# Optimization experiments

Measured on AMD Instinct MI355X. Metric: run time of the kernel, lower is better.

Reference implementation:

```python
import jax, jax.numpy as jnp
import numpy as np

N = 100000   # nodes
E = 1600000  # edges
H = 128      # hidden_dim
B = 4096     # number of root pairs
HOPS = 3


def setup_inputs() -> dict:
    key = jax.random.key(0)
    ks = jax.random.split(key, 12)
    s = 0.05
    return {
        "node_feat": jax.random.normal(ks[0], (N, H), jnp.float32),
        "send_embd": jax.random.normal(ks[1], (N, H), jnp.float32),
        "edge_index": jax.random.randint(ks[2], (2, E), 0, N, dtype=jnp.int32),
        "root_index": jax.random.randint(ks[3], (2 * B,), 0, N, dtype=jnp.int32),
        "agg_by_source": 1,
        "lin1_W": jax.random.normal(ks[4], (2 * H, H), jnp.float32) * s,
        "lin1_b": jnp.zeros((H,), jnp.float32),
        "gat_W": jax.random.normal(ks[5], (HOPS, H, H), jnp.float32) * s,
        "gat_asrc": jax.random.normal(ks[6], (HOPS, H), jnp.float32) * s,
        "gat_adst": jax.random.normal(ks[7], (HOPS, H), jnp.float32) * s,
        "gat_b": jnp.zeros((HOPS, H), jnp.float32),
        "lstm_Wih": jax.random.normal(ks[8], (HOPS, 2 * H, 4 * H), jnp.float32) * s,
        "lstm_Whh": jax.random.normal(ks[9], (HOPS, H, 4 * H), jnp.float32) * s,
        "lstm_b": jnp.zeros((HOPS, 4 * H), jnp.float32),
        "lin2_W": jax.random.normal(ks[10], (H, H), jnp.float32) * s,
        "lin2_b": jnp.zeros((H,), jnp.float32),
    }


def _gat_breadth(x, src, dst, W, a_src, a_dst, b):
    # GATConv(heads=1) followed by tanh (GeniePath Breadth layer)
    xw = x @ W                                  # [N, H]
    e_score = jax.nn.leaky_relu((xw @ a_src)[src] + (xw @ a_dst)[dst], 0.2)  # [E]
    # softmax over incoming edges of each destination node
    m = jax.ops.segment_max(e_score, dst, num_segments=N)
    ex = jnp.exp(e_score - m[dst])
    z = jax.ops.segment_sum(ex, dst, num_segments=N)
    alpha = ex / z[dst]                          # [E]
    agg = jax.ops.segment_sum(alpha[:, None] * xw[src], dst, num_segments=N)
    return jnp.tanh(agg + b)


def _lstm_step(inp, h, c, Wih, Whh, b):
    gates = inp @ Wih + h @ Whh + b              # [N, 4H]
    i, f, g, o = jnp.split(gates, 4, axis=-1)
    c = jax.nn.sigmoid(f) * c + jax.nn.sigmoid(i) * jnp.tanh(g)
    h = jax.nn.sigmoid(o) * jnp.tanh(c)
    return h, c


def reference(node_feat, send_embd, edge_index, root_index, agg_by_source,
              lin1_W, lin1_b, gat_W, gat_asrc, gat_adst, gat_b,
              lstm_Wih, lstm_Whh, lstm_b, lin2_W, lin2_b):
    src, dst = edge_index[0], edge_index[1]
    # Aggregation stage input: concat node embedding with broadcast embedding
    x = jnp.concatenate([node_feat, send_embd], axis=1) @ lin1_W + lin1_b  # [N, H]
    # GeniePathLazy: all breadth (GAT) layers run on the projected input x
    h_tmps = [
        _gat_breadth(x, src, dst, gat_W[i], gat_asrc[i], gat_adst[i], gat_b[i])
        for i in range(HOPS)
    ]
    # Depth: per-node LSTM over the hop axis, input = cat(h_tmp, x_prev)
    h = jnp.zeros_like(x)
    c = jnp.zeros_like(x)
    xs = x
    for i in range(HOPS):
        inp = jnp.concatenate([h_tmps[i], xs], axis=1)   # [N, 2H]
        h, c = _lstm_step(inp, h, c, lstm_Wih[i], lstm_Whh[i], lstm_b[i])
        xs = h
    out = xs @ lin2_W + lin2_b                            # [N, H]
    roots = root_index.reshape(-1, 2)
    src_nodes = roots[:, 0] if agg_by_source else roots[:, 1]
    return out[src_nodes]                                 # [B, H]
```

## Files before the change

### kernel.cpp

```cpp
#include <hip/hip_runtime.h>

constexpr int N  = 100000;
constexpr int E  = 1600000;
constexpr int H  = 128;
constexpr int NB = 4096;
constexpr int HOPS = 3;
constexpr int EPT = 8;

constexpr int WOFF_L1  = 0;
constexpr int WOFF_GAT = 32768;
constexpr int WOFF_CAT = 81920;
constexpr int WOFF_L2  = 671744;
constexpr int WTOT     = 688128;

constexpr size_t ALIGN = 256;
constexpr size_t alup(size_t x) { return (x + ALIGN - 1) & ~(ALIGN - 1); }

constexpr size_t OFF_X       = 0;
constexpr size_t OFF_SSRC    = alup(OFF_X + (size_t)N * H * 4);
constexpr size_t OFF_SDST    = alup(OFF_SSRC + (size_t)3 * N * 4);
constexpr size_t OFF_WVEC    = alup(OFF_SDST + (size_t)3 * N * 4);
constexpr size_t OFF_SELMAP  = alup(OFF_WVEC + 6 * H * 4);
constexpr size_t OFF_NODELST = alup(OFF_SELMAP + (size_t)N * 4);
constexpr size_t OFF_CNT     = alup(OFF_NODELST + NB * 4);
constexpr size_t OFF_DEG     = alup(OFF_CNT + 256);
constexpr size_t OFF_OFFS    = alup(OFF_DEG + NB * 4);
constexpr size_t OFF_CURSOR  = alup(OFF_OFFS + (NB + 1) * 4);
constexpr size_t OFF_ESORT   = alup(OFF_CURSOR + NB * 4);
constexpr size_t OFF_AGGXH   = alup(OFF_ESORT + (size_t)E * 4);
constexpr size_t OFF_AGGXL   = alup(OFF_AGGXH + (size_t)3 * NB * H * 2);
constexpr size_t OFF_XSH     = alup(OFF_AGGXL + (size_t)3 * NB * H * 2);
constexpr size_t OFF_XSL     = alup(OFF_XSH + (size_t)NB * H * 2);
constexpr size_t OFF_L2OUT   = alup(OFF_XSL + (size_t)NB * H * 2);
constexpr size_t OFF_WHI     = alup(OFF_L2OUT + (size_t)NB * H * 4);
constexpr size_t OFF_WLO     = alup(OFF_WHI + (size_t)WTOT * 2);

constexpr size_t OFF_AGGRAW  = OFF_X;
constexpr size_t OFF_WV2     = OFF_X + (size_t)16 * 1024 * 1024;
constexpr size_t OFF_C2      = OFF_WV2 + 6 * 256 * 4;

__device__ __forceinline__ float lrelu(float v) { return v > 0.f ? v : 0.2f * v; }
__device__ __forceinline__ float sigmoidf_(float v) { return 1.f / (1.f + __expf(-v)); }

__device__ __forceinline__ unsigned short f2bf(float f) {
  unsigned u = __float_as_uint(f);
  unsigned r = (u + 0x7FFFu + ((u >> 16) & 1u)) >> 16;
  return (unsigned short)r;
}
__device__ __forceinline__ float bf2f(unsigned short h) {
  return __uint_as_float((unsigned)h << 16);
}
__device__ __forceinline__ void split_rne(float f, unsigned short& hi, unsigned short& lo) {
  unsigned short hh = f2bf(f);
  hi = hh;
  lo = f2bf(f - bf2f(hh));
}
__device__ __forceinline__ void split_trunc(float f, short* hi, short* lo) {
  unsigned u = __float_as_uint(f);
  *hi = (short)(u >> 16);
  float r = f - __uint_as_float(u & 0xFFFF0000u);
  *lo = (short)(__float_as_uint(r) >> 16);
}

typedef short bf16x8 __attribute__((ext_vector_type(8)));
typedef float f32x4  __attribute__((ext_vector_type(4)));

#define MFMA3(ACC, AH, AL, BH, BL)                                               \
  ACC = __builtin_amdgcn_mfma_f32_16x16x32_bf16(AH, BH, ACC, 0, 0, 0);           \
  ACC = __builtin_amdgcn_mfma_f32_16x16x32_bf16(AH, BL, ACC, 0, 0, 0);           \
  ACC = __builtin_amdgcn_mfma_f32_16x16x32_bf16(AL, BH, ACC, 0, 0, 0);

__global__ void init_ws(int* __restrict__ sel_map, int* __restrict__ deg,
                        int* __restrict__ cursor, int* __restrict__ cnt,
                        int* __restrict__ need_flag) {
  int i = blockIdx.x * 256 + threadIdx.x;
  int stride = gridDim.x * 256;
  for (int n = i; n < N; n += stride) { sel_map[n] = -1; need_flag[n] = 0; }
  for (int n = i; n < NB; n += stride) { deg[n] = 0; cursor[n] = 0; }
  if (i < 64) cnt[i] = 0;
}

__global__ void prep_kernel(const float* __restrict__ gat_W,
                            const float* __restrict__ a_src,
                            const float* __restrict__ a_dst,
                            float* __restrict__ wvec,
                            const float* __restrict__ lin1_W,
                            const float* __restrict__ Wih,
                            const float* __restrict__ Whh,
                            const float* __restrict__ lin2_W,
                            unsigned short* __restrict__ whi,
                            unsigned short* __restrict__ wlo) {
  if (blockIdx.x < 6) {
    int i = blockIdx.x >> 1, which = blockIdx.x & 1;
    int k = threadIdx.x;
    __shared__ float av[H];
    if (k < H) av[k] = which ? a_dst[i * H + k] : a_src[i * H + k];
    __syncthreads();
    if (k >= H) return;
    const float* Wr = gat_W + (size_t)i * H * H + (size_t)k * H;
    float s = 0.f;
    #pragma unroll 8
    for (int j = 0; j < H; j++) s = fmaf(Wr[j], av[j], s);
    wvec[(i * 2 + which) * H + k] = s;
    return;
  }
  int idx = (blockIdx.x - 6) * 256 + threadIdx.x;
  if (idx >= WTOT) return;
  float v;
  if (idx < WOFF_GAT) {
    int rel = idx;
    int e = rel & 7, lane = (rel >> 3) & 63, tile = rel >> 9;
    int nl = lane & 15, quad = lane >> 4;
    int c = tile & 7, t = tile >> 3;
    int n = c * 16 + nl, k = t * 32 + quad * 8 + e;
    v = lin1_W[k * 128 + n];
  } else if (idx < WOFF_CAT) {
    int rel = idx - WOFF_GAT;
    int hop = rel / 16384; rel %= 16384;
    int e = rel & 7, lane = (rel >> 3) & 63, tile = rel >> 9;
    int nl = lane & 15, quad = lane >> 4;
    int c = tile & 7, t = tile >> 3;
    int n = c * 16 + nl, k = t * 32 + quad * 8 + e;
    v = gat_W[hop * 16384 + k * 128 + n];
  } else if (idx < WOFF_L2) {
    int rel = idx - WOFF_CAT;
    int hop = rel / 196608; rel %= 196608;
    int e = rel & 7, lane = (rel >> 3) & 63, tile = rel >> 9;
    int nl = lane & 15, quad = lane >> 4;
    int c = tile & 31, t = tile >> 5;
    int ftile = c >> 2, g = c & 3;
    int col = g * 128 + ftile * 16 + nl;
    int k = t * 32 + quad * 8 + e;
    v = (k < 256) ? Wih[hop * 131072 + k * 512 + col]
                  : Whh[hop * 65536 + (k - 256) * 512 + col];
  } else {
    int rel = idx - WOFF_L2;
    int e = rel & 7, lane = (rel >> 3) & 63, tile = rel >> 9;
    int nl = lane & 15, quad = lane >> 4;
    int c = tile & 7, t = tile >> 3;
    int n = c * 16 + nl, k = t * 32 + quad * 8 + e;
    v = lin2_W[k * 128 + n];
  }
  unsigned short hh, ll;
  split_rne(v, hh, ll);
  whi[idx] = hh;
  wlo[idx] = ll;
}

__global__ void prep2_kernel(const float* __restrict__ lin1_W,
                             const float* __restrict__ lin1_b,
                             const float* __restrict__ wvec,
                             float* __restrict__ wv2, float* __restrict__ c2) {
  int v = blockIdx.x;
  int j = threadIdx.x;
  __shared__ float wv[H];
  if (j < H) wv[j] = wvec[v * H + j];
  __syncthreads();
  const float* Wr = lin1_W + (size_t)j * H;
  float s = 0.f;
  #pragma unroll 8
  for (int m = 0; m < H; m++) s = fmaf(Wr[m], wv[m], s);
  wv2[v * 256 + j] = s;
  if (j == 0) {
    float cc = 0.f;
    for (int m = 0; m < H; m++) cc = fmaf(lin1_b[m], wv[m], cc);
    c2[v] = cc;
  }
}

__global__ void roots_assign(const int* __restrict__ root, const int* __restrict__ aggp,
                             int* __restrict__ sel_map, int* __restrict__ node_list,
                             int* __restrict__ cnt, int* __restrict__ need_flag) {
  int b = blockIdx.x * 256 + threadIdx.x;
  if (b >= NB) return;
  int node = root[2 * b + (aggp[0] ? 0 : 1)];
  need_flag[node] = 1;
  int old = atomicCAS(&sel_map[node], -1, -2);
  if (old == -1) {
    int c = atomicAdd(cnt, 1);
    sel_map[node] = c;
    node_list[c] = node;
  }
}

__global__ void count_edges(const int* __restrict__ ei, const int* __restrict__ sel_map,
                            int* __restrict__ deg) {
  const int T = gridDim.x * 256;
  const int base = blockIdx.x * 256 + threadIdx.x;
  int dn[EPT];
  #pragma unroll
  for (int k = 0; k < EPT; k++) {
    int e = base + k * T;
    dn[k] = (e < E) ? ei[E + e] : -1;
  }
  #pragma unroll
  for (int k = 0; k < EPT; k++) {
    if (dn[k] >= 0) dn[k] = sel_map[dn[k]];
  }
  #pragma unroll
  for (int k = 0; k < EPT; k++) {
    if (dn[k] >= 0) atomicAdd(&deg[dn[k]], 1);
  }
}

__global__ __launch_bounds__(1024)
void scan_kernel(const int* __restrict__ deg, int* __restrict__ offs) {
  __shared__ int part[1024];
  int t = threadIdx.x;
  int base = t * 4;
  int v0 = deg[base], v1 = deg[base + 1], v2 = deg[base + 2], v3 = deg[base + 3];
  int s = v0 + v1 + v2 + v3;
  part[t] = s;
  __syncthreads();
  for (int off = 1; off < 1024; off <<= 1) {
    int tmp = (t >= off) ? part[t - off] : 0;
    __syncthreads();
    part[t] += tmp;
    __syncthreads();
  }
  int run = part[t] - s;
  offs[base] = run; run += v0;
  offs[base + 1] = run; run += v1;
  offs[base + 2] = run; run += v2;
  offs[base + 3] = run;
  if (t == 1023) offs[NB] = part[1023];
}

__global__ void scatter_edges2(const int* __restrict__ ei, const int* __restrict__ sel_map,
                               const int* __restrict__ offs, int* __restrict__ cursor,
                               int* __restrict__ es_sorted, int* __restrict__ need_flag) {
  const int T = gridDim.x * 256;
  const int base = blockIdx.x * 256 + threadIdx.x;
  int dn[EPT], sn[EPT];
  #pragma unroll
  for (int k = 0; k < EPT; k++) {
    int e = base + k * T;
    dn[k] = (e < E) ? ei[E + e] : -1;
  }
  #pragma unroll
  for (int k = 0; k < EPT; k++) {
    if (dn[k] >= 0) dn[k] = sel_map[dn[k]];
  }
  #pragma unroll
  for (int k = 0; k < EPT; k++) {
    int e = base + k * T;
    if (dn[k] >= 0) sn[k] = ei[e];
  }
  #pragma unroll
  for (int k = 0; k < EPT; k++) {
    if (dn[k] >= 0) {
      int p = atomicAdd(&cursor[dn[k]], 1);
      es_sorted[offs[dn[k]] + p] = sn[k];
      need_flag[sn[k]] = 1;
    }
  }
}

__global__ void compact_need(const int* __restrict__ need_flag,
                             int* __restrict__ need_list, int* __restrict__ need_cnt) {
  int i = blockIdx.x * 256 + threadIdx.x;
  bool f = (i < N) && (need_flag[i] != 0);
  unsigned long long mask = __ballot(f);
  int lane = threadIdx.x & 63;
  int wcnt = __popcll(mask);
  int base = 0;
  if (lane == 0 && wcnt > 0) base = atomicAdd(need_cnt, wcnt);
  base = __shfl(base, 0);
  if (f) {
    int prefix = __popcll(mask & ((1ull << lane) - 1ull));
    need_list[base + prefix] = i;
  }
}

__global__ __launch_bounds__(256)
void score_pass(const float* __restrict__ a0, const float* __restrict__ a1,
                const float* __restrict__ wv2, const float* __restrict__ c2,
                float* __restrict__ s_src, float* __restrict__ s_dst,
                const int* __restrict__ need_list, const int* __restrict__ need_cnt) {
  const int nneed = need_cnt[0];
  if (blockIdx.x * 16 >= nneed) return;
  __shared__ float Ws[6 * 256];
  __shared__ float C2s[6];
  const int t = threadIdx.x, lane = t & 63, wave = t >> 6;
  const int nl = lane & 15;
  #pragma unroll
  for (int v = 0; v < 6; v++) Ws[v * 256 + t] = wv2[v * 256 + t];
  if (t < 6) C2s[t] = c2[t];
  __syncthreads();

  int r = blockIdx.x * 16 + wave * 4 + (lane >> 4);
  int row = (r < nneed) ? need_list[r] : -1;
  int rc = (row < 0) ? 0 : row;
  const float* src = (nl < 8) ? (a0 + (size_t)rc * H + nl * 16)
                              : (a1 + (size_t)rc * H + (nl - 8) * 16);
  float4 va[4];
  #pragma unroll
  for (int q = 0; q < 4; q++) va[q] = ((const float4*)src)[q];

  float p[6] = {0.f, 0.f, 0.f, 0.f, 0.f, 0.f};
  #pragma unroll
  for (int q = 0; q < 4; q++) {
    float4 v4 = va[q];
    #pragma unroll
    for (int v = 0; v < 6; v++) {
      float4 w4 = *(const float4*)&Ws[v * 256 + nl * 16 + q * 4];
      p[v] = fmaf(v4.x, w4.x, p[v]);
      p[v] = fmaf(v4.y, w4.y, p[v]);
      p[v] = fmaf(v4.z, w4.z, p[v]);
      p[v] = fmaf(v4.w, w4.w, p[v]);
    }
  }
  #pragma unroll
  for (int m = 1; m < 16; m <<= 1)
    #pragma unroll
    for (int v = 0; v < 6; v++) p[v] += __shfl_xor(p[v], m);
  if (nl == 0 && row >= 0) {
    #pragma unroll
    for (int h3 = 0; h3 < 3; h3++) {
      s_src[h3 * N + row] = p[2 * h3 + 0] + C2s[2 * h3 + 0];
      s_dst[h3 * N + row] = p[2 * h3 + 1] + C2s[2 * h3 + 1];
    }
  }
}

__global__ __launch_bounds__(256)
void gat_node_kernel(const int* __restrict__ node_list, const int* __restrict__ cntp,
                     const int* __restrict__ offs, const int* __restrict__ es_sorted,
                     const float* __restrict__ a0, const float* __restrict__ a1,
                     const float* __restrict__ s_src, const float* __restrict__ s_dst,
                     float* __restrict__ agg_raw) {
  int c = blockIdx.x;
  if (c >= cntp[0]) return;
  int t = threadIdx.x;
  int n = node_list[c];
  float sd0 = s_dst[0 * N + n], sd1 = s_dst[1 * N + n], sd2 = s_dst[2 * N + n];
  int e0 = offs[c], e1 = offs[c + 1];
  float m0 = -1e30f, m1 = -1e30f, m2 = -1e30f;
  for (int e = e0 + t; e < e1; e += 256) {
    int s = es_sorted[e];
    m0 = fmaxf(m0, lrelu(s_src[0 * N + s] + sd0));
    m1 = fmaxf(m1, lrelu(s_src[1 * N + s] + sd1));
    m2 = fmaxf(m2, lrelu(s_src[2 * N + s] + sd2));
  }
  __shared__ float red[3][256];
  red[0][t] = m0; red[1][t] = m1; red[2][t] = m2;
  __syncthreads();
  for (int s2 = 128; s2 > 0; s2 >>= 1) {
    if (t < s2) {
      red[0][t] = fmaxf(red[0][t], red[0][t + s2]);
      red[1][t] = fmaxf(red[1][t], red[1][t + s2]);
      red[2][t] = fmaxf(red[2][t], red[2][t + s2]);
    }
    __syncthreads();
  }
  m0 = red[0][0]; m1 = red[1][0]; m2 = red[2][0];
  float u0 = 0.f, u1 = 0.f, u2 = 0.f, z0 = 0.f, z1 = 0.f, z2 = 0.f;
  for (int e = e0; e < e1; e++) {
    int s = es_sorted[e];
    float xs = (t < 128) ? a0[(size_t)s * H + t] : a1[(size_t)s * H + (t - 128)];
    float ex0 = __expf(lrelu(s_src[0 * N + s] + sd0) - m0);
    float ex1 = __expf(lrelu(s_src[1 * N + s] + sd1) - m1);
    float ex2 = __expf(lrelu(s_src[2 * N + s] + sd2) - m2);
    z0 += ex0; z1 += ex1; z2 += ex2;
    u0 = fmaf(ex0, xs, u0); u1 = fmaf(ex1, xs, u1); u2 = fmaf(ex2, xs, u2);
  }
  size_t cb = (size_t)c * 256 + t;
  bool any = e1 > e0;
  agg_raw[0 * ((size_t)NB * 256) + cb] = any ? u0 / z0 : 0.f;
  agg_raw[1 * ((size_t)NB * 256) + cb] = any ? u1 / z1 : 0.f;
  agg_raw[2 * ((size_t)NB * 256) + cb] = any ? u2 / z2 : 0.f;
}

__global__ __launch_bounds__(256)
void gemm_unified(const float* __restrict__ agg_raw,
                  const float* __restrict__ a0, const float* __restrict__ a1,
                  const int* __restrict__ node_list, const int* __restrict__ cntp,
                  const int* __restrict__ offs,
                  const unsigned short* __restrict__ Bth,
                  const unsigned short* __restrict__ Btl,
                  const float* __restrict__ bias,
                  unsigned short* __restrict__ aggxh, unsigned short* __restrict__ aggxl,
                  unsigned short* __restrict__ xsh, unsigned short* __restrict__ xsl) {
  const int t = threadIdx.x, lane = t & 63, wave = t >> 6;
  const int nl = lane & 15, quad = lane >> 4;
  const int rt = blockIdx.x * 64 + wave * 16;
  const int cnt = cntp[0];

  int gr = rt + nl;
  const float *pA, *pB;
  if (gr < 12288) {
    pA = agg_raw + (size_t)gr * 256;
    pB = pA + 128;
  } else {
    int cc = gr - 12288;
    int node = (cc < cnt) ? node_list[cc] : 0;
    pA = a0 + (size_t)node * H;
    pB = a1 + (size_t)node * H;
  }

  f32x4 acc[8];
  #pragma unroll
  for (int c = 0; c < 8; c++) acc[c] = (f32x4){0.f, 0.f, 0.f, 0.f};

  #pragma unroll
  for (int kt = 0; kt < 8; kt++) {
    const float* p = ((kt < 4) ? pA : pB) + (kt & 3) * 32 + quad * 8;
    bf16x8 ahi, alo;
    {
      float4 v0 = *(const float4*)p;
      float4 v1 = *(const float4*)(p + 4);
      float af[8] = {v0.x, v0.y, v0.z, v0.w, v1.x, v1.y, v1.z, v1.w};
      #pragma unroll
      for (int j = 0; j < 8; j++) {
        short h_, l_;
        split_trunc(af[j], &h_, &l_);
        ahi[j] = h_;
        alo[j] = l_;
      }
    }
    #pragma unroll
    for (int c = 0; c < 8; c++) {
      size_t boff = ((size_t)(kt * 8 + c) * 64 + lane) * 8;
      bf16x8 bh = *(const bf16x8*)(Bth + boff);
      bf16x8 bl = *(const bf16x8*)(Btl + boff);
      MFMA3(acc[c], ahi, alo, bh, bl);
    }
  }

  float bv[8];
  #pragma unroll
  for (int c = 0; c < 8; c++) bv[c] = bias[c * 16 + nl];

  #pragma unroll
  for (int r = 0; r < 4; r++) {
    int g2 = rt + quad * 4 + r;
    if (g2 < 12288) {
      int cc = g2 & 4095, h = g2 >> 12;
      bool he = offs[cc + 1] > offs[cc];
      size_t base = (size_t)h * NB * H + (size_t)cc * H;
      #pragma unroll
      for (int c = 0; c < 8; c++) {
        float val = acc[c][r] + (he ? bv[c] : 0.f);
        unsigned short vh, vl;
        split_rne(val, vh, vl);
        aggxh[base + c * 16 + nl] = vh;
        aggxl[base + c * 16 + nl] = vl;
      }
    } else {
      int cc = g2 - 12288;
      size_t base = (size_t)cc * H;
      #pragma unroll
      for (int c = 0; c < 8; c++) {
        float val = acc[c][r] + bv[c];
        unsigned short vh, vl;
        split_rne(val, vh, vl);
        xsh[base + c * 16 + nl] = vh;
        xsl[base + c * 16 + nl] = vl;
      }
    }
  }
}

__global__ __launch_bounds__(512)
void hops3_fused(const unsigned short* __restrict__ aggxh,
                 const unsigned short* __restrict__ aggxl,
                 const unsigned short* __restrict__ xsh,
                 const unsigned short* __restrict__ xsl,
                 const unsigned short* __restrict__ gWh_all,
                 const unsigned short* __restrict__ gWl_all,
                 const float* __restrict__ gbias_all,
                 const unsigned short* __restrict__ CWh_all,
                 const unsigned short* __restrict__ CWl_all,
                 const float* __restrict__ lbias_all,
                 const unsigned short* __restrict__ L2h,
                 const unsigned short* __restrict__ L2l,
                 const float* __restrict__ lin2_b, float* __restrict__ l2out) {
  __shared__ unsigned short Ah[16 * 136], Al[16 * 136];
  __shared__ unsigned short Xh[16 * 136], Xl[16 * 136];
  __shared__ unsigned short Th[16 * 136], Tl[16 * 136];
  __shared__ unsigned short Hh[16 * 136], Hl[16 * 136];
  const int t = threadIdx.x, lane = t & 63, wave = t >> 6;
  const int nl = lane & 15, quad = lane >> 4;
  const int r0 = blockIdx.x * 16;

  for (int i = t; i < 16 * 64; i += 512) {
    int row = i >> 6, c2 = (i & 63) * 2;
    *(ushort2*)&Xh[row * 136 + c2] = *(const ushort2*)&xsh[(size_t)(r0 + row) * H + c2];
    *(ushort2*)&Xl[row * 136 + c2] = *(const ushort2*)&xsl[(size_t)(r0 + row) * H + c2];
  }

  float creg[4] = {0.f, 0.f, 0.f, 0.f};
  const int f = wave * 16 + nl;

  f32x4 acc2[4];
  #pragma unroll
  for (int hop = 0; hop < 3; hop++) {
    const unsigned short* agh = aggxh + (size_t)hop * NB * H;
    const unsigned short* agl = aggxl + (size_t)hop * NB * H;
    __syncthreads();
    for (int i = t; i < 16 * 64; i += 512) {
      int row = i >> 6, c2 = (i & 63) * 2;
      *(ushort2*)&Ah[row * 136 + c2] = *(const ushort2*)&agh[(size_t)(r0 + row) * H + c2];
      *(ushort2*)&Al[row * 136 + c2] = *(const ushort2*)&agl[(size_t)(r0 + row) * H + c2];
    }
    __syncthreads();

    const unsigned short* gWh = gWh_all + hop * 16384;
    const unsigned short* gWl = gWl_all + hop * 16384;
    f32x4 acc1 = (f32x4){0.f, 0.f, 0.f, 0.f};
    #pragma unroll
    for (int kt = 0; kt < 4; kt++) {
      int kk = kt * 32 + quad * 8;
      bf16x8 ah = *(const bf16x8*)&Ah[nl * 136 + kk];
      bf16x8 al = *(const bf16x8*)&Al[nl * 136 + kk];
      size_t boff = ((size_t)(kt * 8 + wave) * 64 + lane) * 8;
      bf16x8 bh = *(const bf16x8*)(gWh + boff);
      bf16x8 bl = *(const bf16x8*)(gWl + boff);
      MFMA3(acc1, ah, al, bh, bl);
    }
    {
      float bv = gbias_all[hop * H + f];
      #pragma unroll
      for (int r = 0; r < 4; r++) {
        int rl = quad * 4 + r;
        float v = tanhf(acc1[r] + bv);
        unsigned short vh, vl2;
        split_rne(v, vh, vl2);
        Th[rl * 136 + f] = vh;
        Tl[rl * 136 + f] = vl2;
      }
    }
    __syncthreads();

    const unsigned short* CWh = CWh_all + hop * 196608;
    const unsigned short* CWl = CWl_all + hop * 196608;
    #pragma unroll
    for (int g = 0; g < 4; g++) acc2[g] = (f32x4){0.f, 0.f, 0.f, 0.f};
    #pragma unroll
    for (int kt = 0; kt < 4; kt++) {
      int kk = kt * 32 + quad * 8;
      bf16x8 ah = *(const bf16x8*)&Th[nl * 136 + kk];
      bf16x8 al = *(const bf16x8*)&Tl[nl * 136 + kk];
      #pragma unroll
      for (int g = 0; g < 4; g++) {
        size_t boff = ((size_t)(kt * 32 + wave * 4 + g) * 64 + lane) * 8;
        bf16x8 bh = *(const bf16x8*)(CWh + boff);
        bf16x8 bl = *(const bf16x8*)(CWl + boff);
        MFMA3(acc2[g], ah, al, bh, bl);
      }
    }
    #pragma unroll
    for (int kt = 0; kt < 4; kt++) {
      int kk = kt * 32 + quad * 8;
      bf16x8 ah, al;
      if (hop == 0) {
        ah = *(const bf16x8*)&Xh[nl * 136 + kk];
        al = *(const bf16x8*)&Xl[nl * 136 + kk];
      } else {
        ah = *(const bf16x8*)&Hh[nl * 136 + kk];
        al = *(const bf16x8*)&Hl[nl * 136 + kk];
      }
      #pragma unroll
      for (int g = 0; g < 4; g++) {
        size_t boff = ((size_t)((kt + 4) * 32 + wave * 4 + g) * 64 + lane) * 8;
        bf16x8 bh = *(const bf16x8*)(CWh + boff);
        bf16x8 bl = *(const bf16x8*)(CWl + boff);
        MFMA3(acc2[g], ah, al, bh, bl);
      }
      if (hop > 0) {
        #pragma unroll
        for (int g = 0; g < 4; g++) {
          size_t boff = ((size_t)((kt + 8) * 32 + wave * 4 + g) * 64 + lane) * 8;
          bf16x8 bh = *(const bf16x8*)(CWh + boff);
          bf16x8 bl = *(const bf16x8*)(CWl + boff);
          MFMA3(acc2[g], ah, al, bh, bl);
        }
      }
    }
    __syncthreads();

    {
      const float* lb = lbias_all + hop * 512;
      float b_i = lb[0 * 128 + f], b_f = lb[1 * 128 + f];
      float b_g = lb[2 * 128 + f], b_o = lb[3 * 128 + f];
      #pragma unroll
      for (int r = 0; r < 4; r++) {
        int rl = quad * 4 + r;
        float gi = acc2[0][r] + b_i;
        float gf = acc2[1][r] + b_f;
        float gg = acc2[2][r] + b_g;
        float go = acc2[3][r] + b_o;
        float cn = sigmoidf_(gf) * creg[r] + sigmoidf_(gi) * tanhf(gg);
        float hn = sigmoidf_(go) * tanhf(cn);
        creg[r] = cn;
        unsigned short vh, vl2;
        split_rne(hn, vh, vl2);
        Hh[rl * 136 + f] = vh;
        Hl[rl * 136 + f] = vl2;
      }
    }
  }
  __syncthreads();

  f32x4 acc3 = (f32x4){0.f, 0.f, 0.f, 0.f};
  #pragma unroll
  for (int kt = 0; kt < 4; kt++) {
    int kk = kt * 32 + quad * 8;
    bf16x8 ah = *(const bf16x8*)&Hh[nl * 136 + kk];
    bf16x8 al = *(const bf16x8*)&Hl[nl * 136 + kk];
    size_t boff = ((size_t)(kt * 8 + wave) * 64 + lane) * 8;
    bf16x8 bh = *(const bf16x8*)(L2h + boff);
    bf16x8 bl = *(const bf16x8*)(L2l + boff);
    MFMA3(acc3, ah, al, bh, bl);
  }
  {
    float bv = lin2_b[f];
    #pragma unroll
    for (int r = 0; r < 4; r++) {
      int row = r0 + quad * 4 + r;
      l2out[(size_t)row * H + f] = acc3[r] + bv;
    }
  }
}

__global__ void scatter_out(const float* __restrict__ l2out, const int* __restrict__ sel_map,
                            const int* __restrict__ root, const int* __restrict__ aggp,
                            float* __restrict__ out) {
  int id = blockIdx.x * 256 + threadIdx.x;
  if (id >= NB * H) return;
  int b = id >> 7, f = id & 127;
  int node = root[2 * b + (aggp[0] ? 0 : 1)];
  int c = sel_map[node];
  out[id] = l2out[(size_t)c * H + f];
}

extern "C" void kernel_launch(void* const* d_in, const int* in_sizes, int n_in,
                              void* d_out, int out_size, void* d_ws, size_t ws_size,
                              hipStream_t stream) {
  const float* node_feat = (const float*)d_in[0];
  const float* send_embd = (const float*)d_in[1];
  const int*   edge_idx  = (const int*)d_in[2];
  const int*   root_idx  = (const int*)d_in[3];
  const int*   aggp      = (const int*)d_in[4];
  const float* lin1_W    = (const float*)d_in[5];
  const float* lin1_b    = (const float*)d_in[6];
  const float* gat_W     = (const float*)d_in[7];
  const float* gat_asrc  = (const float*)d_in[8];
  const float* gat_adst  = (const float*)d_in[9];
  const float* gat_b     = (const float*)d_in[10];
  const float* lstm_Wih  = (const float*)d_in[11];
  const float* lstm_Whh  = (const float*)d_in[12];
  const float* lstm_b    = (const float*)d_in[13];
  const float* lin2_W    = (const float*)d_in[14];
  const float* lin2_b    = (const float*)d_in[15];
  float* out = (float*)d_out;

  char* ws = (char*)d_ws;
  float* agg_raw = (float*)(ws + OFF_AGGRAW);
  float* wv2     = (float*)(ws + OFF_WV2);
  float* c2      = (float*)(ws + OFF_C2);
  float* s_src   = (float*)(ws + OFF_SSRC);
  float* s_dst   = (float*)(ws + OFF_SDST);
  float* wvec    = (float*)(ws + OFF_WVEC);
  int*   sel_map = (int*)(ws + OFF_SELMAP);
  int*   nodelst = (int*)(ws + OFF_NODELST);
  int*   cnt     = (int*)(ws + OFF_CNT);
  int*   deg     = (int*)(ws + OFF_DEG);
  int*   offs    = (int*)(ws + OFF_OFFS);
  int*   cursor  = (int*)(ws + OFF_CURSOR);
  int*   esort   = (int*)(ws + OFF_ESORT);
  unsigned short* aggxh = (unsigned short*)(ws + OFF_AGGXH);
  unsigned short* aggxl = (unsigned short*)(ws + OFF_AGGXL);
  unsigned short* xsh   = (unsigned short*)(ws + OFF_XSH);
  unsigned short* xsl   = (unsigned short*)(ws + OFF_XSL);
  float* l2out   = (float*)(ws + OFF_L2OUT);
  unsigned short* whi = (unsigned short*)(ws + OFF_WHI);
  unsigned short* wlo = (unsigned short*)(ws + OFF_WLO);

  int* need_flag = (int*)(ws + OFF_AGGXH);
  int* need_list = need_flag + N;
  int* need_cnt  = cnt + 1;

  init_ws<<<512, 256, 0, stream>>>(sel_map, deg, cursor, cnt, need_flag);
  prep_kernel<<<6 + (WTOT + 255) / 256, 256, 0, stream>>>(
      gat_W, gat_asrc, gat_adst, wvec, lin1_W, lstm_Wih, lstm_Whh, lin2_W, whi, wlo);
  prep2_kernel<<<6, 256, 0, stream>>>(lin1_W, lin1_b, wvec, wv2, c2);
  roots_assign<<<(NB + 255) / 256, 256, 0, stream>>>(root_idx, aggp, sel_map, nodelst, cnt,
                                                     need_flag);

  const int egrid = (E + 256 * EPT - 1) / (256 * EPT);
  count_edges<<<egrid, 256, 0, stream>>>(edge_idx, sel_map, deg);
  scan_kernel<<<1, 1024, 0, stream>>>(deg, offs);
  scatter_edges2<<<egrid, 256, 0, stream>>>(edge_idx, sel_map, offs, cursor, esort,
                                            need_flag);
  compact_need<<<(N + 255) / 256, 256, 0, stream>>>(need_flag, need_list, need_cnt);

  score_pass<<<(N + 15) / 16, 256, 0, stream>>>(
      node_feat, send_embd, wv2, c2, s_src, s_dst, need_list, need_cnt);

  gat_node_kernel<<<NB, 256, 0, stream>>>(nodelst, cnt, offs, esort,
                                          node_feat, send_embd, s_src, s_dst, agg_raw);

  gemm_unified<<<256, 256, 0, stream>>>(
      agg_raw, node_feat, send_embd, nodelst, cnt, offs,
      whi + WOFF_L1, wlo + WOFF_L1, lin1_b,
      aggxh, aggxl, xsh, xsl);

  hops3_fused<<<NB / 16, 512, 0, stream>>>(
      aggxh, aggxl, xsh, xsl,
      whi + WOFF_GAT, wlo + WOFF_GAT, gat_b,
      whi + WOFF_CAT, wlo + WOFF_CAT, lstm_b,
      whi + WOFF_L2, wlo + WOFF_L2, lin2_b, l2out);

  scatter_out<<<(NB * H + 255) / 256, 256, 0, stream>>>(l2out, sel_map, root_idx, aggp, out);
}
```

Measured before the change: 323.8 us.

## Compact matching edges into packed list and async-prefetch hop tiles via LDS loads

The edge bucketing is restructured. The first pass now also writes each matching (dst-slot, src) pair as a packed int into a compact list and marks the need flags. The second pass then scatters only those pairs instead of rereading and remapping all 1.6M edges. Separately, hops3_fused loads its aggregate and x tiles with global_load_lds into an XOR-swizzled, double-buffered LDS layout, so the next hop's tile is prefetched during compute. The changes add an extra workspace buffer and rely on the packing fitting in 17 bits for the src index and 15 bits for the slot.

```diff
diff --git a/kernel.cpp b/kernel.cpp
--- a/kernel.cpp
+++ b/kernel.cpp
@@ -37,7 +37,8 @@
 
 constexpr size_t OFF_AGGRAW  = OFF_X;
 constexpr size_t OFF_WV2     = OFF_X + (size_t)16 * 1024 * 1024;
-constexpr size_t OFF_C2      = OFF_WV2 + 6 * 256 * 4;
+constexpr size_t OFF_C2     = OFF_WV2 + 6 * 256 * 4;
+constexpr size_t OFF_PLIST  = OFF_X + (size_t)20 * 1024 * 1024;
 
 __device__ __forceinline__ float lrelu(float v) { return v > 0.f ? v : 0.2f * v; }
 __device__ __forceinline__ float sigmoidf_(float v) { return 1.f / (1.f + __expf(-v)); }
@@ -69,6 +70,11 @@
   ACC = __builtin_amdgcn_mfma_f32_16x16x32_bf16(AH, BH, ACC, 0, 0, 0);           \
   ACC = __builtin_amdgcn_mfma_f32_16x16x32_bf16(AH, BL, ACC, 0, 0, 0);           \
   ACC = __builtin_amdgcn_mfma_f32_16x16x32_bf16(AL, BH, ACC, 0, 0, 0);
+
+#define GLOAD_LDS16(G, L)                                                        \
+  __builtin_amdgcn_global_load_lds(                                              \
+      (const __attribute__((address_space(1))) void*)(G),                        \
+      (__attribute__((address_space(3))) void*)(L), 16, 0, 0)
 
 __global__ void init_ws(int* __restrict__ sel_map, int* __restrict__ deg,
                         int* __restrict__ cursor, int* __restrict__ cnt,
@@ -183,11 +189,16 @@
   }
 }
 
-__global__ void count_edges(const int* __restrict__ ei, const int* __restrict__ sel_map,
-                            int* __restrict__ deg) {
+__global__ void edge_pass1(const int* __restrict__ ei, const int* __restrict__ sel_map,
+                           int* __restrict__ deg, int* __restrict__ plist,
+                           int* __restrict__ plist_cnt, int* __restrict__ need_flag) {
+  __shared__ int lcnt, lbase;
   const int T = gridDim.x * 256;
-  const int base = blockIdx.x * 256 + threadIdx.x;
-  int dn[EPT];
+  const int tid = threadIdx.x, lane = tid & 63;
+  if (tid == 0) lcnt = 0;
+  __syncthreads();
+  const int base = blockIdx.x * 256 + tid;
+  int dn[EPT], sn[EPT], pos[EPT];
   #pragma unroll
   for (int k = 0; k < EPT; k++) {
     int e = base + k * T;
@@ -199,7 +210,26 @@
   }
   #pragma unroll
   for (int k = 0; k < EPT; k++) {
-    if (dn[k] >= 0) atomicAdd(&deg[dn[k]], 1);
+    int e = base + k * T;
+    sn[k] = (dn[k] >= 0) ? ei[e] : 0;
+  }
+  #pragma unroll
+  for (int k = 0; k < EPT; k++) {
+    bool f = dn[k] >= 0;
+    if (f) { atomicAdd(&deg[dn[k]], 1); need_flag[sn[k]] = 1; }
+    unsigned long long mask = __ballot(f);
+    int wc = __popcll(mask);
+    int wb = 0;
+    if (lane == 0 && wc > 0) wb = atomicAdd(&lcnt, wc);
+    wb = __shfl(wb, 0);
+    pos[k] = f ? (wb + __popcll(mask & ((1ull << lane) - 1ull))) : -1;
+  }
+  __syncthreads();
+  if (tid == 0) lbase = (lcnt > 0) ? atomicAdd(plist_cnt, lcnt) : 0;
+  __syncthreads();
+  #pragma unroll
+  for (int k = 0; k < EPT; k++) {
+    if (pos[k] >= 0) plist[lbase + pos[k]] = (dn[k] << 17) | sn[k];
   }
 }
 
@@ -226,33 +256,15 @@
   if (t == 1023) offs[NB] = part[1023];
 }
 
-__global__ void scatter_edges2(const int* __restrict__ ei, const int* __restrict__ sel_map,
-                               const int* __restrict__ offs, int* __restrict__ cursor,
-                               int* __restrict__ es_sorted, int* __restrict__ need_flag) {
-  const int T = gridDim.x * 256;
-  const int base = blockIdx.x * 256 + threadIdx.x;
-  int dn[EPT], sn[EPT];
-  #pragma unroll
-  for (int k = 0; k < EPT; k++) {
-    int e = base + k * T;
-    dn[k] = (e < E) ? ei[E + e] : -1;
-  }
-  #pragma unroll
-  for (int k = 0; k < EPT; k++) {
-    if (dn[k] >= 0) dn[k] = sel_map[dn[k]];
-  }
-  #pragma unroll
-  for (int k = 0; k < EPT; k++) {
-    int e = base + k * T;
-    if (dn[k] >= 0) sn[k] = ei[e];
-  }
-  #pragma unroll
-  for (int k = 0; k < EPT; k++) {
-    if (dn[k] >= 0) {
-      int p = atomicAdd(&cursor[dn[k]], 1);
-      es_sorted[offs[dn[k]] + p] = sn[k];
-      need_flag[sn[k]] = 1;
-    }
+__global__ void edge_pass2(const int* __restrict__ plist, const int* __restrict__ plist_cnt,
+                           const int* __restrict__ offs, int* __restrict__ cursor,
+                           int* __restrict__ es_sorted) {
+  int np = plist_cnt[0];
+  for (int i = blockIdx.x * 256 + threadIdx.x; i < np; i += gridDim.x * 256) {
+    int pk = plist[i];
+    int d = pk >> 17, s = pk & 0x1FFFF;
+    int p = atomicAdd(&cursor[d], 1);
+    es_sorted[offs[d] + p] = s;
   }
 }
 
@@ -475,44 +487,48 @@
                  const unsigned short* __restrict__ L2h,
                  const unsigned short* __restrict__ L2l,
                  const float* __restrict__ lin2_b, float* __restrict__ l2out) {
-  __shared__ unsigned short Ah[16 * 136], Al[16 * 136];
-  __shared__ unsigned short Xh[16 * 136], Xl[16 * 136];
+  __shared__ unsigned short Ah[2][2048], Al[2][2048];
+  __shared__ unsigned short Xh[2048], Xl[2048];
   __shared__ unsigned short Th[16 * 136], Tl[16 * 136];
   __shared__ unsigned short Hh[16 * 136], Hl[16 * 136];
   const int t = threadIdx.x, lane = t & 63, wave = t >> 6;
   const int nl = lane & 15, quad = lane >> 4;
   const int r0 = blockIdx.x * 16;
-
-  for (int i = t; i < 16 * 64; i += 512) {
-    int row = i >> 6, c2 = (i & 63) * 2;
-    *(ushort2*)&Xh[row * 136 + c2] = *(const ushort2*)&xsh[(size_t)(r0 + row) * H + c2];
-    *(ushort2*)&Xl[row * 136 + c2] = *(const ushort2*)&xsl[(size_t)(r0 + row) * H + c2];
-  }
+  const int f = wave * 16 + nl;
+
+  const int aj = wave & 3;
+  const bool hiArr = wave < 4;
+  const int ac = aj * 64 + lane;
+  const int arow = ac >> 4, aks = ac & 15;
+  const int akg = aks ^ (arow & 7);
+  const size_t asrc = (size_t)(r0 + arow) * H + akg * 8;
+
+  GLOAD_LDS16((hiArr ? xsh : xsl) + asrc, (hiArr ? Xh : Xl) + aj * 512);
+  GLOAD_LDS16((hiArr ? aggxh : aggxl) + asrc,
+              (hiArr ? &Ah[0][0] : &Al[0][0]) + aj * 512);
+  asm volatile("s_waitcnt vmcnt(0)" ::: "memory");
+  __syncthreads();
 
   float creg[4] = {0.f, 0.f, 0.f, 0.f};
-  const int f = wave * 16 + nl;
-
   f32x4 acc2[4];
+
   #pragma unroll
   for (int hop = 0; hop < 3; hop++) {
-    const unsigned short* agh = aggxh + (size_t)hop * NB * H;
-    const unsigned short* agl = aggxl + (size_t)hop * NB * H;
-    __syncthreads();
-    for (int i = t; i < 16 * 64; i += 512) {
-      int row = i >> 6, c2 = (i & 63) * 2;
-      *(ushort2*)&Ah[row * 136 + c2] = *(const ushort2*)&agh[(size_t)(r0 + row) * H + c2];
-      *(ushort2*)&Al[row * 136 + c2] = *(const ushort2*)&agl[(size_t)(r0 + row) * H + c2];
-    }
-    __syncthreads();
+    const int buf = hop & 1;
+    if (hop < 2) {
+      const unsigned short* sp =
+          (hiArr ? aggxh : aggxl) + (size_t)(hop + 1) * NB * H + asrc;
+      GLOAD_LDS16(sp, (hiArr ? &Ah[buf ^ 1][0] : &Al[buf ^ 1][0]) + aj * 512);
+    }
 
     const unsigned short* gWh = gWh_all + hop * 16384;
     const unsigned short* gWl = gWl_all + hop * 16384;
     f32x4 acc1 = (f32x4){0.f, 0.f, 0.f, 0.f};
     #pragma unroll
     for (int kt = 0; kt < 4; kt++) {
-      int kk = kt * 32 + quad * 8;
-      bf16x8 ah = *(const bf16x8*)&Ah[nl * 136 + kk];
-      bf16x8 al = *(const bf16x8*)&Al[nl * 136 + kk];
+      int sw = ((((kt << 2) + quad) ^ (nl & 7)) << 3);
+      bf16x8 ah = *(const bf16x8*)&Ah[buf][nl * 128 + sw];
+      bf16x8 al = *(const bf16x8*)&Al[buf][nl * 128 + sw];
       size_t boff = ((size_t)(kt * 8 + wave) * 64 + lane) * 8;
       bf16x8 bh = *(const bf16x8*)(gWh + boff);
       bf16x8 bl = *(const bf16x8*)(gWl + boff);
@@ -551,12 +567,13 @@
     }
     #pragma unroll
     for (int kt = 0; kt < 4; kt++) {
-      int kk = kt * 32 + quad * 8;
       bf16x8 ah, al;
       if (hop == 0) {
-        ah = *(const bf16x8*)&Xh[nl * 136 + kk];
-        al = *(const bf16x8*)&Xl[nl * 136 + kk];
+        int sw = ((((kt << 2) + quad) ^ (nl & 7)) << 3);
+        ah = *(const bf16x8*)&Xh[nl * 128 + sw];
+        al = *(const bf16x8*)&Xl[nl * 128 + sw];
       } else {
+        int kk = kt * 32 + quad * 8;
         ah = *(const bf16x8*)&Hh[nl * 136 + kk];
         al = *(const bf16x8*)&Hl[nl * 136 + kk];
       }
@@ -599,8 +616,9 @@
         Hl[rl * 136 + f] = vl2;
       }
     }
-  }
-  __syncthreads();
+    asm volatile("s_waitcnt vmcnt(0)" ::: "memory");
+    __syncthreads();
+  }
 
   f32x4 acc3 = (f32x4){0.f, 0.f, 0.f, 0.f};
   #pragma unroll
@@ -659,6 +677,7 @@
   float* agg_raw = (float*)(ws + OFF_AGGRAW);
   float* wv2     = (float*)(ws + OFF_WV2);
   float* c2      = (float*)(ws + OFF_C2);
+  int*   plist   = (int*)(ws + OFF_PLIST);
   float* s_src   = (float*)(ws + OFF_SSRC);
   float* s_dst   = (float*)(ws + OFF_SDST);
   float* wvec    = (float*)(ws + OFF_WVEC);
@@ -680,6 +699,7 @@
   int* need_flag = (int*)(ws + OFF_AGGXH);
   int* need_list = need_flag + N;
   int* need_cnt  = cnt + 1;
+  int* plist_cnt = cnt + 2;
 
   init_ws<<<512, 256, 0, stream>>>(sel_map, deg, cursor, cnt, need_flag);
   prep_kernel<<<6 + (WTOT + 255) / 256, 256, 0, stream>>>(
@@ -689,11 +709,11 @@
                                                      need_flag);
 
   const int egrid = (E + 256 * EPT - 1) / (256 * EPT);
-  count_edges<<<egrid, 256, 0, stream>>>(edge_idx, sel_map, deg);
+  edge_pass1<<<egrid, 256, 0, stream>>>(edge_idx, sel_map, deg, plist, plist_cnt,
+                                        need_flag);
+  compact_need<<<(N + 255) / 256, 256, 0, stream>>>(need_flag, need_list, need_cnt);
   scan_kernel<<<1, 1024, 0, stream>>>(deg, offs);
-  scatter_edges2<<<egrid, 256, 0, stream>>>(edge_idx, sel_map, offs, cursor, esort,
-                                            need_flag);
-  compact_need<<<(N + 255) / 256, 256, 0, stream>>>(need_flag, need_list, need_cnt);
+  edge_pass2<<<256, 256, 0, stream>>>(plist, plist_cnt, offs, cursor, esort);
 
   score_pass<<<(N + 15) / 16, 256, 0, stream>>>(
       node_feat, send_embd, wv2, c2, s_src, s_dst, need_list, need_cnt);
```

Measured after the change: 321.5 us. About the same (-0.7%).
